# Optimization experiments

Measured on AMD Instinct MI355X. Metric: run time of the kernel, lower is better.

## Reference

```python
import jax, jax.numpy as jnp
import numpy as np

B, N, D = 4, 4096, 256


def setup_inputs() -> dict:
    key = jax.random.key(0)
    k1, k2 = jax.random.split(key)
    val = jax.random.normal(k1, (B, N, D), dtype=jnp.float32)
    state = jax.random.normal(k2, (B, N), dtype=jnp.float32)
    return {"val": val, "state": state}


def reference(val, state):
    # pairwise_fn: scaled dot-product -> scores [B, N, N]
    scale = val.shape[-1] ** -0.5
    scores = jnp.einsum("bid,bjd->bij", val, val) * scale
    # edge_compress_fn = softsign (non-softmax compression)
    edges = scores / (1.0 + jnp.abs(scores))
    # state_weight_edges=False, val/state projections are Identity
    delta_state = jnp.einsum("bij,bj->bi", edges, state)   # [B, N]
    delta_val = jnp.einsum("bij,bjd->bid", edges, val)      # [B, N, D]
    return (delta_state, delta_val)
```

## Files before the change

kernel.cpp:

```cpp
#include <hip/hip_runtime.h>


#define B_  4
#define N_  4096
#define D_  256

typedef __attribute__((ext_vector_type(8))) short short8;
typedef __attribute__((ext_vector_type(4))) float floatx4;

__device__ __forceinline__ unsigned short f2bf(float f) {
    unsigned int u = __float_as_uint(f);
    u += 0x7fff + ((u >> 16) & 1);
    return (unsigned short)(u >> 16);
}

__device__ __forceinline__ void gl_lds16(const void* g, void* l) {
    __builtin_amdgcn_global_load_lds(
        (const __attribute__((address_space(1))) unsigned int*)g,
        (__attribute__((address_space(3))) unsigned int*)l, 16, 0, 0);
}
__device__ __forceinline__ void gl_lds4(const void* g, void* l) {
    __builtin_amdgcn_global_load_lds(
        (const __attribute__((address_space(1))) unsigned int*)g,
        (__attribute__((address_space(3))) unsigned int*)l, 4, 0, 0);
}

__global__ __launch_bounds__(256)
void prepass_kernel(const float* __restrict__ val,
                    unsigned short* __restrict__ Vb,
                    unsigned short* __restrict__ VT) {
    __shared__ unsigned short tile[64][68];
    const int t   = threadIdx.x;
    const int blk = blockIdx.x;
    const int b   = blk >> 8;
    const int it  = (blk >> 2) & 63;
    const int dt  = blk & 3;
    const int i0  = it * 64, d0 = dt * 64;
    const float*    vb  = val + (size_t)b * N_ * D_;
    unsigned short* Vbb = Vb  + (size_t)b * N_ * D_;
    unsigned short* VTb = VT  + (size_t)b * D_ * N_;

    #pragma unroll
    for (int q = 0; q < 4; ++q) {
        int idx = t + 256 * q;
        int row = idx >> 4;
        int c4  = idx & 15;
        float4 v = *(const float4*)(vb + (size_t)(i0 + row) * D_ + d0 + c4 * 4);
        ushort4 h;
        h.x = f2bf(v.x); h.y = f2bf(v.y); h.z = f2bf(v.z); h.w = f2bf(v.w);
        *(ushort4*)(Vbb + (size_t)(i0 + row) * D_ + d0 + c4 * 4) = h;
        *(ushort4*)&tile[row][c4 * 4] = h;
    }
    __syncthreads();
    #pragma unroll
    for (int q = 0; q < 4; ++q) {
        int dr = (t >> 4) + q * 16;
        int i4 = t & 15;
        ushort4 h;
        h.x = tile[i4 * 4 + 0][dr];
        h.y = tile[i4 * 4 + 1][dr];
        h.z = tile[i4 * 4 + 2][dr];
        h.w = tile[i4 * 4 + 3][dr];
        *(ushort4*)(VTb + (size_t)(d0 + dr) * N_ + i0 + i4 * 4) = h;
    }
}

__global__ __launch_bounds__(512, 1)
void prop_main(const float* __restrict__ state,
               const unsigned short* __restrict__ Vb,
               const unsigned short* __restrict__ VT,
               float* __restrict__ dvp,
               float* __restrict__ dsp_o)
{
    __shared__ __attribute__((aligned(16))) unsigned char smem[136448];

    const int t    = threadIdx.x;
    const int g    = t >> 8;
    const int w    = t >> 6;
    const int w4   = w & 3;
    const int lane = t & 63;
    const int quad = lane >> 4;
    const int l16  = lane & 15;

    const int x   = blockIdx.x;
    const int b   = x >> 6;
    const int it  = (x >> 1) & 31;
    const int jh  = x & 1;
    const int it0 = it * 128;
    const int jbase = jh * 2048;
    const int niter = 32;

    unsigned short* vjL  = (unsigned short*)(smem + 65536);
    unsigned short* stjL_= (unsigned short*)(smem + 135168);
    float*          stjL = (float*)stjL_;
    float*          dsredg = (float*)(smem + 135424 + g * 512);

    const unsigned short* Vbb = Vb + (size_t)b * N_ * D_;
    const unsigned short* VTb = VT + (size_t)b * D_ * N_;
    const float*          stb = state + (size_t)b * N_;

    const int hi  = lane >> 5;
    const int p32 = lane & 31;
    const int dr8 = lane >> 3;
    const int p8  = lane & 7;

    int vgoff[4];
    int tgoff[4];
    #pragma unroll
    for (int n = 0; n < 4; ++n) {
        int r  = 2 * (w * 4 + n) + hi;
        int gr = p32 ^ (r & 7);
        vgoff[n] = r * 256 + gr * 8;
        int d  = 8 * (w * 4 + n) + dr8;
        int gt = p8 ^ dr8;
        tgoff[n] = d * 4096 + gt * 8;
    }

    const int r0 = (w4 >> 1) * 32;
    const int c0 = (w4 & 1) * 32;
    const int pA = l16 & 7;

    short8 A0[8], A1[8];
    {
        const unsigned short* ar0 = Vbb + (size_t)(it0 + g * 64 + r0 + l16) * 256 + quad * 8;
        const unsigned short* ar1 = ar0 + 16 * 256;
        #pragma unroll
        for (int ks = 0; ks < 8; ++ks) {
            A0[ks] = *(const short8*)(ar0 + ks * 32);
            A1[ks] = *(const short8*)(ar1 + ks * 32);
        }
    }

    #pragma unroll
    for (int n = 0; n < 4; ++n)
        gl_lds16(VTb + (size_t)jbase + tgoff[n],
                 smem + (w * 4 + n) * 1024);
    #pragma unroll
    for (int n = 0; n < 4; ++n)
        gl_lds16(Vbb + (size_t)jbase * 256 + vgoff[n],
                 smem + 65536 + (w * 4 + n) * 1024);
    if (w == 0) gl_lds4(stb + jbase + lane, stjL);

    floatx4 dv[4][4];
    #pragma unroll
    for (int a = 0; a < 4; ++a)
        #pragma unroll
        for (int c = 0; c < 4; ++c)
            dv[a][c] = (floatx4){0.f, 0.f, 0.f, 0.f};
    float dsp[8];
    #pragma unroll
    for (int k = 0; k < 8; ++k) dsp[k] = 0.f;

    for (int k = 0; k < niter; ++k) {
        const int buf = k & 1;
        unsigned short* Eshg = (unsigned short*)(smem + 98304 + g * 18432 + buf * 9216);
        unsigned short* vjtg = (unsigned short*)(smem + buf * 32768);

        __syncthreads();

        if (k + 1 < niter) {
            const size_t j0n = jbase + (size_t)(k + 1) * 64;
            #pragma unroll
            for (int n = 0; n < 4; ++n)
                gl_lds16(VTb + j0n + tgoff[n],
                         smem + (buf ^ 1) * 32768 + (w * 4 + n) * 1024);
        }

        floatx4 sa[2][2];
        #pragma unroll
        for (int a = 0; a < 2; ++a)
            #pragma unroll
            for (int c = 0; c < 2; ++c)
                sa[a][c] = (floatx4){0.f, 0.f, 0.f, 0.f};

        #pragma unroll
        for (int ks = 0; ks < 8; ++ks) {
            const int p = ((ks * 4 + quad) ^ pA) * 8;
            short8 b0 = *(const short8*)&vjL[(c0 + l16) * 256 + p];
            short8 b1 = *(const short8*)&vjL[(c0 + 16 + l16) * 256 + p];
            sa[0][0] = __builtin_amdgcn_mfma_f32_16x16x32_bf16(A0[ks], b0, sa[0][0], 0, 0, 0);
            sa[0][1] = __builtin_amdgcn_mfma_f32_16x16x32_bf16(A0[ks], b1, sa[0][1], 0, 0, 0);
            sa[1][0] = __builtin_amdgcn_mfma_f32_16x16x32_bf16(A1[ks], b0, sa[1][0], 0, 0, 0);
            sa[1][1] = __builtin_amdgcn_mfma_f32_16x16x32_bf16(A1[ks], b1, sa[1][1], 0, 0, 0);
        }

        float stc0 = stjL[c0 + l16];
        float stc1 = stjL[c0 + 16 + l16];
        #pragma unroll
        for (int a = 0; a < 2; ++a) {
            #pragma unroll
            for (int r = 0; r < 4; ++r) {
                const int il = r0 + a * 16 + quad * 4 + r;
                float s0 = sa[a][0][r];
                float s1 = sa[a][1][r];
                float e0 = s0 * __builtin_amdgcn_rcpf(16.0f + fabsf(s0));
                float e1 = s1 * __builtin_amdgcn_rcpf(16.0f + fabsf(s1));
                dsp[a * 4 + r] += e0 * stc0 + e1 * stc1;
                Eshg[il * 72 + c0 + l16]      = f2bf(e0);
                Eshg[il * 72 + c0 + 16 + l16] = f2bf(e1);
            }
        }
        __syncthreads();

        if (k + 1 < niter) {
            const size_t j0n = jbase + (size_t)(k + 1) * 64;
            #pragma unroll
            for (int n = 0; n < 4; ++n)
                gl_lds16(Vbb + j0n * 256 + vgoff[n],
                         smem + 65536 + (w * 4 + n) * 1024);
            if (w == 0) gl_lds4(stb + j0n + lane, stjL);
        }

        #pragma unroll
        for (int ks = 0; ks < 2; ++ks) {
            short8 af[4], bfr[4];
            #pragma unroll
            for (int a2 = 0; a2 < 4; ++a2)
                af[a2] = *(const short8*)&Eshg[(a2 * 16 + l16) * 72 + ks * 32 + quad * 8];
            #pragma unroll
            for (int c2 = 0; c2 < 4; ++c2) {
                const int d = w4 * 64 + c2 * 16 + l16;
                const int p = ((ks * 4 + quad) ^ (l16 & 7)) * 8;
                bfr[c2] = *(const short8*)&vjtg[d * 64 + p];
            }
            #pragma unroll
            for (int a2 = 0; a2 < 4; ++a2)
                #pragma unroll
                for (int c2 = 0; c2 < 4; ++c2)
                    dv[a2][c2] = __builtin_amdgcn_mfma_f32_16x16x32_bf16(af[a2], bfr[c2], dv[a2][c2], 0, 0, 0);
        }
    }

    float* dvo = dvp + (size_t)jh * B_ * N_ * D_ + (size_t)b * N_ * D_
                     + (size_t)(it0 + g * 64) * D_;
    #pragma unroll
    for (int a2 = 0; a2 < 4; ++a2)
        #pragma unroll
        for (int c2 = 0; c2 < 4; ++c2)
            #pragma unroll
            for (int r = 0; r < 4; ++r) {
                const int il = a2 * 16 + quad * 4 + r;
                const int d  = w4 * 64 + c2 * 16 + l16;
                dvo[(size_t)il * D_ + d] = dv[a2][c2][r];
            }

    #pragma unroll
    for (int k = 0; k < 8; ++k) {
        float v = dsp[k];
        v += __shfl_xor(v, 1);
        v += __shfl_xor(v, 2);
        v += __shfl_xor(v, 4);
        v += __shfl_xor(v, 8);
        dsp[k] = v;
    }
    if (l16 == 0) {
        #pragma unroll
        for (int a = 0; a < 2; ++a)
            #pragma unroll
            for (int r = 0; r < 4; ++r) {
                const int row = r0 + a * 16 + quad * 4 + r;
                dsredg[(w4 & 1) * 64 + row] = dsp[a * 4 + r];
            }
    }
    __syncthreads();
    if (t < 128) {
        const int gg  = t >> 6;
        const int row = t & 63;
        const float* dsr = (const float*)(smem + 135424 + gg * 512);
        dsp_o[(size_t)jh * B_ * N_ + (size_t)b * N_ + it0 + gg * 64 + row]
            = dsr[row] + dsr[64 + row];
    }
}

__global__ __launch_bounds__(256)
void combine_kernel(const float4* __restrict__ dv0, const float4* __restrict__ dv1,
                    const float*  __restrict__ ds0, const float*  __restrict__ ds1,
                    float* __restrict__ out) {
    const int NDV4 = B_ * N_ * D_ / 4;
    const int NDS  = B_ * N_;
    int x = blockIdx.x * 256 + threadIdx.x;
    if (x < NDV4) {
        float4 a = dv0[x], c = dv1[x];
        float4 r;
        r.x = a.x + c.x; r.y = a.y + c.y; r.z = a.z + c.z; r.w = a.w + c.w;
        ((float4*)(out + NDS))[x] = r;
    } else {
        int y = (x - NDV4) * 4;
        if (y < NDS) {
            float4 a = *(const float4*)(ds0 + y);
            float4 c = *(const float4*)(ds1 + y);
            float4 r;
            r.x = a.x + c.x; r.y = a.y + c.y; r.z = a.z + c.z; r.w = a.w + c.w;
            *(float4*)(out + y) = r;
        }
    }
}

__global__ __launch_bounds__(256, 1)
void prop_kernel_fb(const float* __restrict__ val,
                    const float* __restrict__ state,
                    float* __restrict__ out) {
    __shared__ __attribute__((aligned(16))) unsigned short vi[64][264];
    __shared__ __attribute__((aligned(16))) unsigned short vj[64][264];
    __shared__ __attribute__((aligned(16))) unsigned short vjt[2048][8];
    __shared__ __attribute__((aligned(16))) unsigned short Esh[64][72];
    __shared__ float stj[64];
    __shared__ float dsred[2][64];

    const int t    = threadIdx.x;
    const int w    = t >> 6;
    const int lane = t & 63;
    const int quad = lane >> 4;
    const int l16  = lane & 15;
    const int b   = blockIdx.x >> 6;
    const int it0 = (blockIdx.x & 63) << 6;
    const float* valb = val   + (size_t)b * N_ * D_;
    const float* stb  = state + (size_t)b * N_;

    #pragma unroll
    for (int n = 0; n < 16; ++n) {
        int idx = t + 256 * n;
        int row = idx >> 6;
        int c4  = idx & 63;
        float4 v = *(const float4*)(valb + (size_t)(it0 + row) * D_ + c4 * 4);
        ushort4 h;
        h.x = f2bf(v.x); h.y = f2bf(v.y); h.z = f2bf(v.z); h.w = f2bf(v.w);
        *(ushort4*)&vi[row][c4 * 4] = h;
    }

    const int r0 = (w >> 1) * 32;
    const int c0 = (w & 1) * 32;
    floatx4 dv[4][4];
    #pragma unroll
    for (int a = 0; a < 4; ++a)
        #pragma unroll
        for (int c = 0; c < 4; ++c)
            dv[a][c] = (floatx4){0.f, 0.f, 0.f, 0.f};
    float dsp[8];
    #pragma unroll
    for (int k = 0; k < 8; ++k) dsp[k] = 0.f;

    for (int jt = 0; jt < 64; ++jt) {
        const int j0 = jt * 64;
        #pragma unroll
        for (int n = 0; n < 16; ++n) {
            int idx = t + 256 * n;
            int row = idx >> 6;
            int c4  = idx & 63;
            float4 v = *(const float4*)(valb + (size_t)(j0 + row) * D_ + c4 * 4);
            ushort4 h;
            h.x = f2bf(v.x); h.y = f2bf(v.y); h.z = f2bf(v.z); h.w = f2bf(v.w);
            *(ushort4*)&vj[row][c4 * 4] = h;
        }
        if (t < 64) stj[t] = stb[j0 + t];
        __syncthreads();

        #pragma unroll
        for (int n = 0; n < 8; ++n) {
            const int d  = t;
            const int jb = n;
            short8 pk;
            #pragma unroll
            for (int jj = 0; jj < 8; ++jj) pk[jj] = (short)vj[jb * 8 + jj][d];
            *(short8*)&vjt[d * 8 + (jb ^ (d & 7))][0] = pk;
        }

        floatx4 sa[2][2];
        #pragma unroll
        for (int a = 0; a < 2; ++a)
            #pragma unroll
            for (int c = 0; c < 2; ++c)
                sa[a][c] = (floatx4){0.f, 0.f, 0.f, 0.f};
        #pragma unroll
        for (int ks = 0; ks < 8; ++ks) {
            const int d0 = ks * 32 + quad * 8;
            short8 a0 = *(const short8*)&vi[r0 + l16][d0];
            short8 a1 = *(const short8*)&vi[r0 + 16 + l16][d0];
            short8 b0 = *(const short8*)&vj[c0 + l16][d0];
            short8 b1 = *(const short8*)&vj[c0 + 16 + l16][d0];
            sa[0][0] = __builtin_amdgcn_mfma_f32_16x16x32_bf16(a0, b0, sa[0][0], 0, 0, 0);
            sa[0][1] = __builtin_amdgcn_mfma_f32_16x16x32_bf16(a0, b1, sa[0][1], 0, 0, 0);
            sa[1][0] = __builtin_amdgcn_mfma_f32_16x16x32_bf16(a1, b0, sa[1][0], 0, 0, 0);
            sa[1][1] = __builtin_amdgcn_mfma_f32_16x16x32_bf16(a1, b1, sa[1][1], 0, 0, 0);
        }

        float stc0 = stj[c0 + l16];
        float stc1 = stj[c0 + 16 + l16];
        #pragma unroll
        for (int a = 0; a < 2; ++a) {
            #pragma unroll
            for (int r = 0; r < 4; ++r) {
                const int il = r0 + a * 16 + quad * 4 + r;
                float s0 = sa[a][0][r] * 0.0625f;
                float s1 = sa[a][1][r] * 0.0625f;
                float e0 = s0 / (1.0f + fabsf(s0));
                float e1 = s1 / (1.0f + fabsf(s1));
                dsp[a * 4 + r] += e0 * stc0 + e1 * stc1;
                Esh[il][c0 + l16]      = f2bf(e0);
                Esh[il][c0 + 16 + l16] = f2bf(e1);
            }
        }
        __syncthreads();

        #pragma unroll
        for (int ks = 0; ks < 2; ++ks) {
            short8 af[4], bfr[4];
            #pragma unroll
            for (int a2 = 0; a2 < 4; ++a2)
                af[a2] = *(const short8*)&Esh[a2 * 16 + l16][ks * 32 + quad * 8];
            #pragma unroll
            for (int c2 = 0; c2 < 4; ++c2) {
                const int d  = w * 64 + c2 * 16 + l16;
                const int jb = ks * 4 + quad;
                bfr[c2] = *(const short8*)&vjt[d * 8 + (jb ^ (d & 7))][0];
            }
            #pragma unroll
            for (int a2 = 0; a2 < 4; ++a2)
                #pragma unroll
                for (int c2 = 0; c2 < 4; ++c2)
                    dv[a2][c2] = __builtin_amdgcn_mfma_f32_16x16x32_bf16(af[a2], bfr[c2], dv[a2][c2], 0, 0, 0);
        }
    }

    float* dvo = out + (size_t)B_ * N_ + (size_t)b * N_ * D_;
    #pragma unroll
    for (int a2 = 0; a2 < 4; ++a2)
        #pragma unroll
        for (int c2 = 0; c2 < 4; ++c2)
            #pragma unroll
            for (int r = 0; r < 4; ++r) {
                const int i = it0 + a2 * 16 + quad * 4 + r;
                const int d = w * 64 + c2 * 16 + l16;
                dvo[(size_t)i * D_ + d] = dv[a2][c2][r];
            }

    #pragma unroll
    for (int k = 0; k < 8; ++k) {
        float v = dsp[k];
        v += __shfl_xor(v, 1);
        v += __shfl_xor(v, 2);
        v += __shfl_xor(v, 4);
        v += __shfl_xor(v, 8);
        dsp[k] = v;
    }
    if (l16 == 0) {
        #pragma unroll
        for (int a = 0; a < 2; ++a)
            #pragma unroll
            for (int r = 0; r < 4; ++r) {
                const int row = (w >> 1) * 32 + a * 16 + quad * 4 + r;
                dsred[w & 1][row] = dsp[a * 4 + r];
            }
    }
    __syncthreads();
    if (t < 64) out[(size_t)b * N_ + it0 + t] = dsred[0][t] + dsred[1][t];
}

extern "C" void kernel_launch(void* const* d_in, const int* in_sizes, int n_in,
                              void* d_out, int out_size, void* d_ws, size_t ws_size,
                              hipStream_t stream) {
    const float* val   = (const float*)d_in[0];
    const float* state = (const float*)d_in[1];
    float* out = (float*)d_out;

    const size_t nE         = (size_t)B_ * N_ * D_;
    const size_t need_base  = 2 * nE * sizeof(unsigned short);
    const size_t need_split = need_base + 2 * nE * sizeof(float)
                            + 2 * (size_t)B_ * N_ * sizeof(float);

    if (ws_size >= need_split) {
        unsigned short* Vb = (unsigned short*)d_ws;
        unsigned short* VT = Vb + nE;
        float* dvp = (float*)(VT + nE);
        float* dsp = dvp + 2 * nE;
        prepass_kernel<<<dim3(1024), dim3(256), 0, stream>>>(val, Vb, VT);
        prop_main<<<dim3(256), dim3(512), 0, stream>>>(state, Vb, VT, dvp, dsp);
        const int NDV4 = B_ * N_ * D_ / 4;
        const int NDS4 = B_ * N_ / 4;
        combine_kernel<<<dim3((NDV4 + NDS4) / 256), dim3(256), 0, stream>>>(
            (const float4*)dvp, (const float4*)(dvp + nE),
            dsp, dsp + (size_t)B_ * N_, out);
    } else {
        prop_kernel_fb<<<dim3(256), dim3(256), 0, stream>>>(val, state, out);
    }
}
```

Before: 151.0 us.

## Keep softsign edges in registers via transposed MFMA and lane shuffles, skipping LDS staging

The first GEMM is transposed so each wave holds the score tile as S^T. The bf16 edges are then repacked into A-operand fragments with cross-lane shuffles, so they no longer go through a shared-memory E tile. Each wave now accumulates its own 32 rows across all 256 D columns, and paired waves reduce their partial dv through LDS at the end. Both V and V^T plus state are double-buffered and prefetched together, which cuts the loop to one barrier per iteration. The cost is more accumulator registers (128 floats per lane), extra shuffles, and an epilogue reduction through LDS.

```diff
diff --git a/kernel.cpp b/kernel.cpp
--- a/kernel.cpp
+++ b/kernel.cpp
@@ -72,7 +72,7 @@
                float* __restrict__ dvp,
                float* __restrict__ dsp_o)
 {
-    __shared__ __attribute__((aligned(16))) unsigned char smem[136448];
+    __shared__ __attribute__((aligned(16))) unsigned char smem[134144];
 
     const int t    = threadIdx.x;
     const int g    = t >> 8;
@@ -90,11 +90,6 @@
     const int jbase = jh * 2048;
     const int niter = 32;
 
-    unsigned short* vjL  = (unsigned short*)(smem + 65536);
-    unsigned short* stjL_= (unsigned short*)(smem + 135168);
-    float*          stjL = (float*)stjL_;
-    float*          dsredg = (float*)(smem + 135424 + g * 512);
-
     const unsigned short* Vbb = Vb + (size_t)b * N_ * D_;
     const unsigned short* VTb = VT + (size_t)b * D_ * N_;
     const float*          stb = state + (size_t)b * N_;
@@ -109,11 +104,9 @@
     #pragma unroll
     for (int n = 0; n < 4; ++n) {
         int r  = 2 * (w * 4 + n) + hi;
-        int gr = p32 ^ (r & 7);
-        vgoff[n] = r * 256 + gr * 8;
+        vgoff[n] = r * 256 + (p32 ^ (r & 7)) * 8;
         int d  = 8 * (w * 4 + n) + dr8;
-        int gt = p8 ^ dr8;
-        tgoff[n] = d * 4096 + gt * 8;
+        tgoff[n] = d * 4096 + (p8 ^ dr8) * 8;
     }
 
     const int r0 = (w4 >> 1) * 32;
@@ -133,39 +126,42 @@
 
     #pragma unroll
     for (int n = 0; n < 4; ++n)
-        gl_lds16(VTb + (size_t)jbase + tgoff[n],
-                 smem + (w * 4 + n) * 1024);
+        gl_lds16(Vbb + (size_t)jbase * 256 + vgoff[n], smem + (w * 4 + n) * 1024);
     #pragma unroll
     for (int n = 0; n < 4; ++n)
-        gl_lds16(Vbb + (size_t)jbase * 256 + vgoff[n],
-                 smem + 65536 + (w * 4 + n) * 1024);
-    if (w == 0) gl_lds4(stb + jbase + lane, stjL);
-
-    floatx4 dv[4][4];
-    #pragma unroll
-    for (int a = 0; a < 4; ++a)
-        #pragma unroll
-        for (int c = 0; c < 4; ++c)
-            dv[a][c] = (floatx4){0.f, 0.f, 0.f, 0.f};
-    float dsp[8];
-    #pragma unroll
-    for (int k = 0; k < 8; ++k) dsp[k] = 0.f;
+        gl_lds16(VTb + (size_t)jbase + tgoff[n], smem + 65536 + (w * 4 + n) * 1024);
+    if (w == 0) gl_lds4(stb + jbase + lane, smem + 131072);
+    __syncthreads();
+
+    floatx4 dv[2][16];
+    #pragma unroll
+    for (int ic = 0; ic < 2; ++ic)
+        #pragma unroll
+        for (int dt = 0; dt < 16; ++dt)
+            dv[ic][dt] = (floatx4){0.f, 0.f, 0.f, 0.f};
+    float dsp[2] = {0.f, 0.f};
+
+    const int src0 = (((2 * quad)     & 3) * 16) + l16;
+    const int src1 = (((2 * quad + 1) & 3) * 16) + l16;
 
     for (int k = 0; k < niter; ++k) {
         const int buf = k & 1;
-        unsigned short* Eshg = (unsigned short*)(smem + 98304 + g * 18432 + buf * 9216);
-        unsigned short* vjtg = (unsigned short*)(smem + buf * 32768);
-
-        __syncthreads();
 
         if (k + 1 < niter) {
             const size_t j0n = jbase + (size_t)(k + 1) * 64;
+            const int nb = buf ^ 1;
+            #pragma unroll
+            for (int n = 0; n < 4; ++n)
+                gl_lds16(Vbb + j0n * 256 + vgoff[n],
+                         smem + nb * 32768 + (w * 4 + n) * 1024);
             #pragma unroll
             for (int n = 0; n < 4; ++n)
                 gl_lds16(VTb + j0n + tgoff[n],
-                         smem + (buf ^ 1) * 32768 + (w * 4 + n) * 1024);
-        }
-
+                         smem + 65536 + nb * 32768 + (w * 4 + n) * 1024);
+            if (w == 0) gl_lds4(stb + j0n + lane, smem + 131072 + nb * 256);
+        }
+
+        const unsigned short* vjb = (const unsigned short*)(smem + buf * 32768);
         floatx4 sa[2][2];
         #pragma unroll
         for (int a = 0; a < 2; ++a)
@@ -176,99 +172,114 @@
         #pragma unroll
         for (int ks = 0; ks < 8; ++ks) {
             const int p = ((ks * 4 + quad) ^ pA) * 8;
-            short8 b0 = *(const short8*)&vjL[(c0 + l16) * 256 + p];
-            short8 b1 = *(const short8*)&vjL[(c0 + 16 + l16) * 256 + p];
-            sa[0][0] = __builtin_amdgcn_mfma_f32_16x16x32_bf16(A0[ks], b0, sa[0][0], 0, 0, 0);
-            sa[0][1] = __builtin_amdgcn_mfma_f32_16x16x32_bf16(A0[ks], b1, sa[0][1], 0, 0, 0);
-            sa[1][0] = __builtin_amdgcn_mfma_f32_16x16x32_bf16(A1[ks], b0, sa[1][0], 0, 0, 0);
-            sa[1][1] = __builtin_amdgcn_mfma_f32_16x16x32_bf16(A1[ks], b1, sa[1][1], 0, 0, 0);
-        }
-
-        float stc0 = stjL[c0 + l16];
-        float stc1 = stjL[c0 + 16 + l16];
-        #pragma unroll
-        for (int a = 0; a < 2; ++a) {
-            #pragma unroll
-            for (int r = 0; r < 4; ++r) {
-                const int il = r0 + a * 16 + quad * 4 + r;
-                float s0 = sa[a][0][r];
-                float s1 = sa[a][1][r];
-                float e0 = s0 * __builtin_amdgcn_rcpf(16.0f + fabsf(s0));
-                float e1 = s1 * __builtin_amdgcn_rcpf(16.0f + fabsf(s1));
-                dsp[a * 4 + r] += e0 * stc0 + e1 * stc1;
-                Eshg[il * 72 + c0 + l16]      = f2bf(e0);
-                Eshg[il * 72 + c0 + 16 + l16] = f2bf(e1);
+            short8 a0 = *(const short8*)&vjb[(c0 + l16) * 256 + p];
+            short8 a1 = *(const short8*)&vjb[(c0 + 16 + l16) * 256 + p];
+            sa[0][0] = __builtin_amdgcn_mfma_f32_16x16x32_bf16(a0, A0[ks], sa[0][0], 0, 0, 0);
+            sa[0][1] = __builtin_amdgcn_mfma_f32_16x16x32_bf16(a0, A1[ks], sa[0][1], 0, 0, 0);
+            sa[1][0] = __builtin_amdgcn_mfma_f32_16x16x32_bf16(a1, A0[ks], sa[1][0], 0, 0, 0);
+            sa[1][1] = __builtin_amdgcn_mfma_f32_16x16x32_bf16(a1, A1[ks], sa[1][1], 0, 0, 0);
+        }
+
+        const float* stjf = (const float*)(smem + 131072 + buf * 256);
+        float4 st0 = *(const float4*)&stjf[c0 + quad * 4];
+        float4 st1 = *(const float4*)&stjf[c0 + 16 + quad * 4];
+        unsigned int P[2][2][2];
+        #pragma unroll
+        for (int ja = 0; ja < 2; ++ja) {
+            #pragma unroll
+            for (int ic = 0; ic < 2; ++ic) {
+                float e0 = sa[ja][ic][0] * __builtin_amdgcn_rcpf(16.0f + fabsf(sa[ja][ic][0]));
+                float e1 = sa[ja][ic][1] * __builtin_amdgcn_rcpf(16.0f + fabsf(sa[ja][ic][1]));
+                float e2 = sa[ja][ic][2] * __builtin_amdgcn_rcpf(16.0f + fabsf(sa[ja][ic][2]));
+                float e3 = sa[ja][ic][3] * __builtin_amdgcn_rcpf(16.0f + fabsf(sa[ja][ic][3]));
+                const float4 st = ja ? st1 : st0;
+                dsp[ic] += e0 * st.x + e1 * st.y + e2 * st.z + e3 * st.w;
+                P[ja][ic][0] = (unsigned int)f2bf(e0) | ((unsigned int)f2bf(e1) << 16);
+                P[ja][ic][1] = (unsigned int)f2bf(e2) | ((unsigned int)f2bf(e3) << 16);
             }
         }
+
+        short8 Af[2];
+        #pragma unroll
+        for (int ic = 0; ic < 2; ++ic) {
+            int lo0 = __shfl((int)P[0][ic][0], src0);
+            int hi0 = __shfl((int)P[1][ic][0], src0);
+            int lo1 = __shfl((int)P[0][ic][1], src0);
+            int hi1 = __shfl((int)P[1][ic][1], src0);
+            int lo2 = __shfl((int)P[0][ic][0], src1);
+            int hi2 = __shfl((int)P[1][ic][0], src1);
+            int lo3 = __shfl((int)P[0][ic][1], src1);
+            int hi3 = __shfl((int)P[1][ic][1], src1);
+            int4 fw;
+            fw.x = (quad < 2) ? lo0 : hi0;
+            fw.y = (quad < 2) ? lo1 : hi1;
+            fw.z = (quad < 2) ? lo2 : hi2;
+            fw.w = (quad < 2) ? lo3 : hi3;
+            Af[ic] = *(short8*)&fw;
+        }
+
+        const unsigned short* vjtb = (const unsigned short*)(smem + 65536 + buf * 32768);
+        #pragma unroll
+        for (int dt = 0; dt < 16; ++dt) {
+            const int pos = (((c0 >> 3) + quad) ^ pA) * 8;
+            short8 bfr = *(const short8*)&vjtb[(dt * 16 + l16) * 64 + pos];
+            dv[0][dt] = __builtin_amdgcn_mfma_f32_16x16x32_bf16(Af[0], bfr, dv[0][dt], 0, 0, 0);
+            dv[1][dt] = __builtin_amdgcn_mfma_f32_16x16x32_bf16(Af[1], bfr, dv[1][dt], 0, 0, 0);
+        }
+
         __syncthreads();
-
-        if (k + 1 < niter) {
-            const size_t j0n = jbase + (size_t)(k + 1) * 64;
-            #pragma unroll
-            for (int n = 0; n < 4; ++n)
-                gl_lds16(Vbb + j0n * 256 + vgoff[n],
-                         smem + 65536 + (w * 4 + n) * 1024);
-            if (w == 0) gl_lds4(stb + j0n + lane, stjL);
-        }
-
-        #pragma unroll
-        for (int ks = 0; ks < 2; ++ks) {
-            short8 af[4], bfr[4];
-            #pragma unroll
-            for (int a2 = 0; a2 < 4; ++a2)
-                af[a2] = *(const short8*)&Eshg[(a2 * 16 + l16) * 72 + ks * 32 + quad * 8];
-            #pragma unroll
-            for (int c2 = 0; c2 < 4; ++c2) {
-                const int d = w4 * 64 + c2 * 16 + l16;
-                const int p = ((ks * 4 + quad) ^ (l16 & 7)) * 8;
-                bfr[c2] = *(const short8*)&vjtg[d * 64 + p];
-            }
-            #pragma unroll
-            for (int a2 = 0; a2 < 4; ++a2)
+    }
+
+    #pragma unroll
+    for (int ic = 0; ic < 2; ++ic) {
+        float v = dsp[ic];
+        v += __shfl_xor(v, 16);
+        v += __shfl_xor(v, 32);
+        dsp[ic] = v;
+    }
+    float* dsred = (float*)(smem + 133120);
+    if (quad == 0) {
+        #pragma unroll
+        for (int ic = 0; ic < 2; ++ic)
+            dsred[g * 128 + (w4 & 1) * 64 + r0 + ic * 16 + l16] = dsp[ic];
+    }
+
+    float* dump = (float*)smem;
+    const int pair = g * 2 + (w4 >> 1);
+    if (w4 & 1) {
+        #pragma unroll
+        for (int ic = 0; ic < 2; ++ic)
+            #pragma unroll
+            for (int dt = 0; dt < 16; ++dt)
                 #pragma unroll
-                for (int c2 = 0; c2 < 4; ++c2)
-                    dv[a2][c2] = __builtin_amdgcn_mfma_f32_16x16x32_bf16(af[a2], bfr[c2], dv[a2][c2], 0, 0, 0);
-        }
-    }
-
-    float* dvo = dvp + (size_t)jh * B_ * N_ * D_ + (size_t)b * N_ * D_
-                     + (size_t)(it0 + g * 64) * D_;
-    #pragma unroll
-    for (int a2 = 0; a2 < 4; ++a2)
-        #pragma unroll
-        for (int c2 = 0; c2 < 4; ++c2)
-            #pragma unroll
-            for (int r = 0; r < 4; ++r) {
-                const int il = a2 * 16 + quad * 4 + r;
-                const int d  = w4 * 64 + c2 * 16 + l16;
-                dvo[(size_t)il * D_ + d] = dv[a2][c2][r];
-            }
-
-    #pragma unroll
-    for (int k = 0; k < 8; ++k) {
-        float v = dsp[k];
-        v += __shfl_xor(v, 1);
-        v += __shfl_xor(v, 2);
-        v += __shfl_xor(v, 4);
-        v += __shfl_xor(v, 8);
-        dsp[k] = v;
-    }
-    if (l16 == 0) {
-        #pragma unroll
-        for (int a = 0; a < 2; ++a)
-            #pragma unroll
-            for (int r = 0; r < 4; ++r) {
-                const int row = r0 + a * 16 + quad * 4 + r;
-                dsredg[(w4 & 1) * 64 + row] = dsp[a * 4 + r];
-            }
+                for (int r = 0; r < 4; ++r) {
+                    const int i32 = ic * 16 + quad * 4 + r;
+                    const int d   = dt * 16 + l16;
+                    dump[pair * 8320 + i32 * 260 + d] = dv[ic][dt][r];
+                }
     }
     __syncthreads();
+
+    if (!(w4 & 1)) {
+        float* dvo = dvp + (size_t)jh * B_ * N_ * D_ + (size_t)b * N_ * D_
+                         + (size_t)(it0 + g * 64 + r0) * D_;
+        #pragma unroll
+        for (int ic = 0; ic < 2; ++ic)
+            #pragma unroll
+            for (int dt = 0; dt < 16; ++dt)
+                #pragma unroll
+                for (int r = 0; r < 4; ++r) {
+                    const int i32 = ic * 16 + quad * 4 + r;
+                    const int d   = dt * 16 + l16;
+                    dvo[(size_t)i32 * D_ + d] =
+                        dv[ic][dt][r] + dump[pair * 8320 + i32 * 260 + d];
+                }
+    }
     if (t < 128) {
-        const int gg  = t >> 6;
-        const int row = t & 63;
-        const float* dsr = (const float*)(smem + 135424 + gg * 512);
-        dsp_o[(size_t)jh * B_ * N_ + (size_t)b * N_ + it0 + gg * 64 + row]
-            = dsr[row] + dsr[64 + row];
+        const int gg = t >> 6;
+        const int i  = t & 63;
+        dsp_o[(size_t)jh * B_ * N_ + (size_t)b * N_ + it0 + gg * 64 + i]
+            = dsred[gg * 128 + i] + dsred[gg * 128 + 64 + i];
     }
 }
 
```

Measured after the change: 185.8 us. 23.0% more time.

## Transpose score MFMA so each wave owns 16 j-columns over all 64 rows

Applied to the files above, without the earlier changes.

Recasts the score GEMM so each wave loads one j-fragment from LDS and multiplies it against four register-resident i-row blocks, producing transposed score tiles. This halves the LDS B-fragment reads per MFMA, lets the softsign output be packed into 64-bit bf16 stores, and loads the state as a single float4. The row-sum reduction becomes a cross-quad shuffle followed by a four-way LDS sum. The register footprint for the i-operands doubles, and launch_bounds is changed to 2 blocks per CU, which cannot actually fit given the roughly 137KB of shared memory per block.

```diff
diff --git a/kernel.cpp b/kernel.cpp
--- a/kernel.cpp
+++ b/kernel.cpp
@@ -65,14 +65,14 @@
     }
 }
 
-__global__ __launch_bounds__(512, 1)
+__global__ __launch_bounds__(512, 2)
 void prop_main(const float* __restrict__ state,
                const unsigned short* __restrict__ Vb,
                const unsigned short* __restrict__ VT,
                float* __restrict__ dvp,
                float* __restrict__ dsp_o)
 {
-    __shared__ __attribute__((aligned(16))) unsigned char smem[136448];
+    __shared__ __attribute__((aligned(16))) unsigned char smem[137472];
 
     const int t    = threadIdx.x;
     const int g    = t >> 8;
@@ -91,9 +91,8 @@
     const int niter = 32;
 
     unsigned short* vjL  = (unsigned short*)(smem + 65536);
-    unsigned short* stjL_= (unsigned short*)(smem + 135168);
-    float*          stjL = (float*)stjL_;
-    float*          dsredg = (float*)(smem + 135424 + g * 512);
+    float*          stjL = (float*)(smem + 135168);
+    float*          dsredg = (float*)(smem + 135424 + g * 1024);
 
     const unsigned short* Vbb = Vb + (size_t)b * N_ * D_;
     const unsigned short* VTb = VT + (size_t)b * D_ * N_;
@@ -109,32 +108,27 @@
     #pragma unroll
     for (int n = 0; n < 4; ++n) {
         int r  = 2 * (w * 4 + n) + hi;
-        int gr = p32 ^ (r & 7);
-        vgoff[n] = r * 256 + gr * 8;
+        vgoff[n] = r * 256 + (p32 ^ (r & 7)) * 8;
         int d  = 8 * (w * 4 + n) + dr8;
-        int gt = p8 ^ dr8;
-        tgoff[n] = d * 4096 + gt * 8;
-    }
-
-    const int r0 = (w4 >> 1) * 32;
-    const int c0 = (w4 & 1) * 32;
+        tgoff[n] = d * 4096 + (p8 ^ dr8) * 8;
+    }
+
+    const int jq = w4 * 16;
     const int pA = l16 & 7;
 
-    short8 A0[8], A1[8];
-    {
-        const unsigned short* ar0 = Vbb + (size_t)(it0 + g * 64 + r0 + l16) * 256 + quad * 8;
-        const unsigned short* ar1 = ar0 + 16 * 256;
-        #pragma unroll
-        for (int ks = 0; ks < 8; ++ks) {
-            A0[ks] = *(const short8*)(ar0 + ks * 32);
-            A1[ks] = *(const short8*)(ar1 + ks * 32);
-        }
+    short8 Vi4[4][8];
+    #pragma unroll
+    for (int ib = 0; ib < 4; ++ib) {
+        const unsigned short* ar =
+            Vbb + (size_t)(it0 + g * 64 + ib * 16 + l16) * 256 + quad * 8;
+        #pragma unroll
+        for (int ks = 0; ks < 8; ++ks)
+            Vi4[ib][ks] = *(const short8*)(ar + ks * 32);
     }
 
     #pragma unroll
     for (int n = 0; n < 4; ++n)
-        gl_lds16(VTb + (size_t)jbase + tgoff[n],
-                 smem + (w * 4 + n) * 1024);
+        gl_lds16(VTb + (size_t)jbase + tgoff[n], smem + (w * 4 + n) * 1024);
     #pragma unroll
     for (int n = 0; n < 4; ++n)
         gl_lds16(Vbb + (size_t)jbase * 256 + vgoff[n],
@@ -147,9 +141,7 @@
         #pragma unroll
         for (int c = 0; c < 4; ++c)
             dv[a][c] = (floatx4){0.f, 0.f, 0.f, 0.f};
-    float dsp[8];
-    #pragma unroll
-    for (int k = 0; k < 8; ++k) dsp[k] = 0.f;
+    float dsp[4] = {0.f, 0.f, 0.f, 0.f};
 
     for (int k = 0; k < niter; ++k) {
         const int buf = k & 1;
@@ -166,39 +158,33 @@
                          smem + (buf ^ 1) * 32768 + (w * 4 + n) * 1024);
         }
 
-        floatx4 sa[2][2];
-        #pragma unroll
-        for (int a = 0; a < 2; ++a)
-            #pragma unroll
-            for (int c = 0; c < 2; ++c)
-                sa[a][c] = (floatx4){0.f, 0.f, 0.f, 0.f};
+        floatx4 sa[4];
+        #pragma unroll
+        for (int ib = 0; ib < 4; ++ib)
+            sa[ib] = (floatx4){0.f, 0.f, 0.f, 0.f};
 
         #pragma unroll
         for (int ks = 0; ks < 8; ++ks) {
             const int p = ((ks * 4 + quad) ^ pA) * 8;
-            short8 b0 = *(const short8*)&vjL[(c0 + l16) * 256 + p];
-            short8 b1 = *(const short8*)&vjL[(c0 + 16 + l16) * 256 + p];
-            sa[0][0] = __builtin_amdgcn_mfma_f32_16x16x32_bf16(A0[ks], b0, sa[0][0], 0, 0, 0);
-            sa[0][1] = __builtin_amdgcn_mfma_f32_16x16x32_bf16(A0[ks], b1, sa[0][1], 0, 0, 0);
-            sa[1][0] = __builtin_amdgcn_mfma_f32_16x16x32_bf16(A1[ks], b0, sa[1][0], 0, 0, 0);
-            sa[1][1] = __builtin_amdgcn_mfma_f32_16x16x32_bf16(A1[ks], b1, sa[1][1], 0, 0, 0);
-        }
-
-        float stc0 = stjL[c0 + l16];
-        float stc1 = stjL[c0 + 16 + l16];
-        #pragma unroll
-        for (int a = 0; a < 2; ++a) {
-            #pragma unroll
-            for (int r = 0; r < 4; ++r) {
-                const int il = r0 + a * 16 + quad * 4 + r;
-                float s0 = sa[a][0][r];
-                float s1 = sa[a][1][r];
-                float e0 = s0 * __builtin_amdgcn_rcpf(16.0f + fabsf(s0));
-                float e1 = s1 * __builtin_amdgcn_rcpf(16.0f + fabsf(s1));
-                dsp[a * 4 + r] += e0 * stc0 + e1 * stc1;
-                Eshg[il * 72 + c0 + l16]      = f2bf(e0);
-                Eshg[il * 72 + c0 + 16 + l16] = f2bf(e1);
-            }
+            short8 aj = *(const short8*)&vjL[(jq + l16) * 256 + p];
+            sa[0] = __builtin_amdgcn_mfma_f32_16x16x32_bf16(aj, Vi4[0][ks], sa[0], 0, 0, 0);
+            sa[1] = __builtin_amdgcn_mfma_f32_16x16x32_bf16(aj, Vi4[1][ks], sa[1], 0, 0, 0);
+            sa[2] = __builtin_amdgcn_mfma_f32_16x16x32_bf16(aj, Vi4[2][ks], sa[2], 0, 0, 0);
+            sa[3] = __builtin_amdgcn_mfma_f32_16x16x32_bf16(aj, Vi4[3][ks], sa[3], 0, 0, 0);
+        }
+
+        float4 st4 = *(const float4*)&stjL[jq + quad * 4];
+        #pragma unroll
+        for (int ib = 0; ib < 4; ++ib) {
+            float e0 = sa[ib][0] * __builtin_amdgcn_rcpf(16.0f + fabsf(sa[ib][0]));
+            float e1 = sa[ib][1] * __builtin_amdgcn_rcpf(16.0f + fabsf(sa[ib][1]));
+            float e2 = sa[ib][2] * __builtin_amdgcn_rcpf(16.0f + fabsf(sa[ib][2]));
+            float e3 = sa[ib][3] * __builtin_amdgcn_rcpf(16.0f + fabsf(sa[ib][3]));
+            dsp[ib] += e0 * st4.x + e1 * st4.y + e2 * st4.z + e3 * st4.w;
+            uint2 pk;
+            pk.x = (unsigned int)f2bf(e0) | ((unsigned int)f2bf(e1) << 16);
+            pk.y = (unsigned int)f2bf(e2) | ((unsigned int)f2bf(e3) << 16);
+            *(uint2*)&Eshg[(ib * 16 + l16) * 72 + jq + quad * 4] = pk;
         }
         __syncthreads();
 
@@ -220,7 +206,7 @@
             #pragma unroll
             for (int c2 = 0; c2 < 4; ++c2) {
                 const int d = w4 * 64 + c2 * 16 + l16;
-                const int p = ((ks * 4 + quad) ^ (l16 & 7)) * 8;
+                const int p = ((ks * 4 + quad) ^ pA) * 8;
                 bfr[c2] = *(const short8*)&vjtg[d * 64 + p];
             }
             #pragma unroll
@@ -245,30 +231,24 @@
             }
 
     #pragma unroll
-    for (int k = 0; k < 8; ++k) {
-        float v = dsp[k];
-        v += __shfl_xor(v, 1);
-        v += __shfl_xor(v, 2);
-        v += __shfl_xor(v, 4);
-        v += __shfl_xor(v, 8);
-        dsp[k] = v;
-    }
-    if (l16 == 0) {
-        #pragma unroll
-        for (int a = 0; a < 2; ++a)
-            #pragma unroll
-            for (int r = 0; r < 4; ++r) {
-                const int row = r0 + a * 16 + quad * 4 + r;
-                dsredg[(w4 & 1) * 64 + row] = dsp[a * 4 + r];
-            }
+    for (int ib = 0; ib < 4; ++ib) {
+        float v = dsp[ib];
+        v += __shfl_xor(v, 16);
+        v += __shfl_xor(v, 32);
+        dsp[ib] = v;
+    }
+    if (quad == 0) {
+        #pragma unroll
+        for (int ib = 0; ib < 4; ++ib)
+            dsredg[w4 * 64 + ib * 16 + l16] = dsp[ib];
     }
     __syncthreads();
     if (t < 128) {
-        const int gg  = t >> 6;
-        const int row = t & 63;
-        const float* dsr = (const float*)(smem + 135424 + gg * 512);
-        dsp_o[(size_t)jh * B_ * N_ + (size_t)b * N_ + it0 + gg * 64 + row]
-            = dsr[row] + dsr[64 + row];
+        const int gg = t >> 6;
+        const int i  = t & 63;
+        const float* dsr = (const float*)(smem + 135424 + gg * 1024);
+        dsp_o[(size_t)jh * B_ * N_ + (size_t)b * N_ + it0 + gg * 64 + i]
+            = dsr[i] + dsr[64 + i] + dsr[128 + i] + dsr[192 + i];
     }
 }
 
```

After: 186.2 us. 1.23x slower.
